# Kernel optimization log

Measured on AMD Instinct MI355X. Metric: run time of the kernel, lower is better.

The kernel has to match this reference:

```python
import jax, jax.numpy as jnp
import numpy as np
import math

B, S, DIN, DQ, DV = 8, 2048, 1024, 1024, 1024


def setup_inputs() -> dict:
    key = jax.random.key(0)
    ks = jax.random.split(key, 9)
    c_q = math.sqrt(6.0 / (DIN + DQ))
    c_v = math.sqrt(6.0 / (DIN + DV))
    query = jax.random.normal(ks[0], (B, S, DIN), dtype=jnp.float32)
    key_t = jax.random.normal(ks[1], (B, S, DIN), dtype=jnp.float32)
    value = jax.random.normal(ks[2], (B, S, DIN), dtype=jnp.float32)
    # Linear weights stored as [in, out] for x @ W; uniform init per module
    Wq = jax.random.uniform(ks[3], (DIN, DQ), jnp.float32, -c_q, c_q)
    Wk = jax.random.uniform(ks[4], (DIN, DQ), jnp.float32, -c_q, c_q)
    Wv = jax.random.uniform(ks[5], (DIN, DV), jnp.float32, -c_v, c_v)
    bq = jax.random.uniform(ks[6], (DQ,), jnp.float32, -c_q, c_q)
    bk = jax.random.uniform(ks[7], (DQ,), jnp.float32, -c_q, c_q)
    bv = jax.random.uniform(ks[8], (DV,), jnp.float32, -c_v, c_v)
    # causal mask: True where attention is disallowed (masked_fill semantics)
    mask = jnp.broadcast_to(jnp.triu(jnp.ones((S, S), dtype=bool), k=1), (B, S, S))
    return {"query": query, "key": key_t, "value": value,
            "Wq": Wq, "bq": bq, "Wk": Wk, "bk": bk, "Wv": Wv, "bv": bv,
            "mask": mask}


def reference(query, key, value, Wq, bq, Wk, bk, Wv, bv, mask):
    q = query @ Wq + bq                       # [B,S,DQ]
    k = key @ Wk + bk                         # [B,S,DQ]
    v = value @ Wv + bv                       # [B,S,DV]
    scores = jnp.einsum('bsd,btd->bst', q, k) / math.sqrt(DQ)  # [B,S,S]
    scores = jnp.where(mask, jnp.float32(-1e9), scores)
    weights = jax.nn.softmax(scores, axis=2)
    y = jnp.einsum('bst,btd->bsd', weights, v)  # [B,S,DV]
    return y
```

## Files before the change

kernel.cpp:

```cpp
#include <hip/hip_runtime.h>


typedef unsigned short u16;
typedef unsigned int   u32;
typedef float f32x4 __attribute__((ext_vector_type(4)));
typedef short s16x8 __attribute__((ext_vector_type(8)));

__device__ __forceinline__ u16 f2bf(float x) {
  u32 u = __builtin_bit_cast(u32, x);
  u += 0x7fffu + ((u >> 16) & 1u);
  return (u16)(u >> 16);
}
__device__ __forceinline__ float bf2f(u16 h) {
  u32 u = (u32)h << 16;
  return __builtin_bit_cast(float, u);
}

__device__ __forceinline__ void gld_lds16(const u16* g, u16* l) {
  __builtin_amdgcn_global_load_lds((const __attribute__((address_space(1))) void*)g,
                                   (__attribute__((address_space(3))) void*)l,
                                   16, 0, 0);
}

__global__ __launch_bounds__(256) void cvt_bf16_3(const float* __restrict__ i0,
                                                  const float* __restrict__ i1,
                                                  const float* __restrict__ i2,
                                                  u16* __restrict__ out, long X) {
  const float* in = blockIdx.y == 0 ? i0 : (blockIdx.y == 1 ? i1 : i2);
  long i = (long)blockIdx.x * 256 + threadIdx.x;
  float4 v = ((const float4*)in)[i];
  ushort4 o;
  o.x = f2bf(v.x); o.y = f2bf(v.y); o.z = f2bf(v.z); o.w = f2bf(v.w);
  ((ushort4*)(out + blockIdx.y * X))[i] = o;
}

__global__ __launch_bounds__(256) void transpose_w3(const float* __restrict__ w0,
                                                    const float* __restrict__ w1,
                                                    const float* __restrict__ w2,
                                                    u16* __restrict__ Wt,
                                                    int K, int N, long WN) {
  __shared__ u16 t[32][33];
  const float* W = blockIdx.z == 0 ? w0 : (blockIdx.z == 1 ? w1 : w2);
  u16* out = Wt + blockIdx.z * WN;
  int n0 = blockIdx.x * 32, k0 = blockIdx.y * 32;
  int tx = threadIdx.x & 31, ty = threadIdx.x >> 5;
  for (int r = ty; r < 32; r += 8)
    t[r][tx] = f2bf(W[(long)(k0 + r) * N + n0 + tx]);
  __syncthreads();
  for (int r = ty; r < 32; r += 8)
    out[(long)(n0 + r) * K + k0 + tx] = t[tx][r];
}

__global__ __launch_bounds__(256) void transpose_v(const u16* __restrict__ v,
                                                   u16* __restrict__ vt,
                                                   int S, int D) {
  __shared__ u16 t[32][33];
  long b = blockIdx.z;
  const u16* vb = v + b * S * D;
  u16* vtb = vt + b * S * D;
  int d0 = blockIdx.x * 32, s0 = blockIdx.y * 32;
  int tx = threadIdx.x & 31, ty = threadIdx.x >> 5;
  for (int r = ty; r < 32; r += 8)
    t[r][tx] = vb[(long)(s0 + r) * D + d0 + tx];
  __syncthreads();
  for (int r = ty; r < 32; r += 8)
    vtb[(long)(d0 + r) * S + s0 + tx] = t[tx][r];
}

__device__ __forceinline__ void gemm_core(const u16* __restrict__ At,
                                          const u16* __restrict__ Bt,
                                          int lda, int ldb, int ktEnd,
                                          f32x4 (&acc)[4][4],
                                          u16* lA, u16* lB) {
  const int tid = threadIdx.x;
  const int lane = tid & 63, half = lane >> 4, l16 = lane & 15;
  const int wave = tid >> 6;
  const int wm = (wave >> 1) * 64, wn = (wave & 1) * 64;

  const int c0 = tid, c1 = tid + 256;
  const int r0 = c0 >> 2, kp0 = (c0 & 3) ^ ((c0 >> 3) & 3);
  const int r1 = c1 >> 2, kp1 = (c1 & 3) ^ ((c1 >> 3) & 3);
  const u16* gA0 = At + (long)r0 * lda + kp0 * 8;
  const u16* gA1 = At + (long)r1 * lda + kp1 * 8;
  const u16* gB0 = Bt + (long)r0 * ldb + kp0 * 8;
  const u16* gB1 = Bt + (long)r1 * ldb + kp1 * 8;
  u16* lA0 = lA + c0 * 8; u16* lA1 = lA + c1 * 8;
  u16* lB0 = lB + c0 * 8; u16* lB1 = lB + c1 * 8;
  const int swz = (half ^ ((l16 >> 1) & 3)) * 8;

  for (int kt = 0; kt < ktEnd; ++kt) {
    const int k0 = kt * 32;
    gld_lds16(gA0 + k0, lA0);
    gld_lds16(gA1 + k0, lA1);
    gld_lds16(gB0 + k0, lB0);
    gld_lds16(gB1 + k0, lB1);
    __syncthreads();
    s16x8 af[4], bfr[4];
#pragma unroll
    for (int mi = 0; mi < 4; ++mi)
      af[mi] = *(const s16x8*)&lA[(wm + mi * 16 + l16) * 32 + swz];
#pragma unroll
    for (int ni = 0; ni < 4; ++ni)
      bfr[ni] = *(const s16x8*)&lB[(wn + ni * 16 + l16) * 32 + swz];
#pragma unroll
    for (int mi = 0; mi < 4; ++mi)
#pragma unroll
      for (int ni = 0; ni < 4; ++ni)
        acc[mi][ni] = __builtin_amdgcn_mfma_f32_16x16x32_bf16(af[mi], bfr[ni], acc[mi][ni], 0, 0, 0);
    __syncthreads();
  }
}

struct ProjPtrs {
  const u16* A[3];
  const u16* B[3];
  u16* C[3];
  const float* bias[3];
};

__global__ __launch_bounds__(512, 2)
void gemm_proj(ProjPtrs p) {
  const int NT = 16;
  const int NIT = 8;
  const int f = blockIdx.x;
  const int wg = (f & 7) * 96 + (f >> 3);
  const int bz = wg >> 8;
  const int rr = wg & 255;
  const int bm = rr >> 2, bn = rr & 3;

  __shared__ u16 lds[65536];
  u16* lA = lds;
  u16* lB = lds + 32768;

  const int tid = threadIdx.x;
  const int lane = tid & 63, l16 = lane & 15, lq = lane >> 4;
  const int w = tid >> 6;

  const u16* At = p.A[bz] + (long)bm * 256 * 1024;
  const u16* Bt = p.B[bz] + (long)bn * 256 * 1024;

  const int sr = tid >> 3;
  const int sc = (tid & 7) ^ (sr & 7);
  const long sO0 = (long)sr * 1024 + sc * 8;
  const int swz0 = ((lq) ^ (l16 & 7)) * 8;
  const int swz1 = ((4 + lq) ^ (l16 & 7)) * 8;
  const int aBase = (w >> 2) * 8192 + l16 * 64;
  const int bBase = ((w & 3) >> 1) * 8192 + (((w & 3) & 1) * 64 + l16) * 64;

  f32x4 acc[8][4];
#pragma unroll
  for (int i = 0; i < 8; ++i)
#pragma unroll
    for (int j = 0; j < 4; ++j) { f32x4 z = {0.f, 0.f, 0.f, 0.f}; acc[i][j] = z; }

  s16x8 af[4], bf0[4], bf1[4];

#define STG(ldsM, gM, buf, h, kt) {                               \
    u16* d_ = (ldsM) + (buf) * 16384 + (h) * 8192 + tid * 8;      \
    const u16* s_ = (gM) + (long)(h) * 131072 + (long)(kt) * 64;  \
    gld_lds16(s_ + sO0, d_);                                      \
    gld_lds16(s_ + sO0 + 65536, d_ + 4096); }
#define RD_AF(BUF, MH, SWZ)                                       \
    _Pragma("unroll") for (int mi = 0; mi < 4; ++mi)              \
      af[mi] = *(const s16x8*)&lA[(BUF) * 16384 + aBase + ((MH) * 4 + mi) * 1024 + (SWZ)];
#define RD_BF(BUF, BF, SWZ)                                       \
    _Pragma("unroll") for (int ni = 0; ni < 4; ++ni)              \
      BF[ni] = *(const s16x8*)&lB[(BUF) * 16384 + bBase + ni * 1024 + (SWZ)];
#define COMPUTE(MH, BF)                                           \
    __builtin_amdgcn_sched_barrier(0);                            \
    __builtin_amdgcn_s_barrier();                                 \
    asm volatile("s_waitcnt lgkmcnt(0)" ::: "memory");            \
    __builtin_amdgcn_sched_barrier(0);                            \
    __builtin_amdgcn_s_setprio(1);                                \
    _Pragma("unroll") for (int mi = 0; mi < 4; ++mi)              \
      _Pragma("unroll") for (int ni = 0; ni < 4; ++ni)            \
        acc[(MH) * 4 + mi][ni] = __builtin_amdgcn_mfma_f32_16x16x32_bf16(af[mi], BF[ni], acc[(MH) * 4 + mi][ni], 0, 0, 0); \
    __builtin_amdgcn_s_setprio(0);
#define ENDPH __builtin_amdgcn_s_barrier();
#define VM2 asm volatile("s_waitcnt vmcnt(2)" ::: "memory");
#define VM0 asm volatile("s_waitcnt vmcnt(0)" ::: "memory");

  STG(lB, Bt, 0, 0, 0); STG(lB, Bt, 0, 1, 0);
  STG(lA, At, 0, 0, 0); STG(lA, At, 0, 1, 0);
  STG(lB, Bt, 1, 0, 1);
  VM2;
  __builtin_amdgcn_s_barrier();

  for (int i = 0; i < NIT; ++i) {
    const int ta = 2 * i, tb = 2 * i + 1;
    const bool st = (i < NIT - 1);
    RD_AF(0, 0, swz0); RD_BF(0, bf0, swz0); STG(lB, Bt, 1, 1, tb);
    COMPUTE(0, bf0); ENDPH;
    RD_AF(0, 1, swz0); STG(lA, At, 1, 0, tb);
    COMPUTE(1, bf0); ENDPH;
    RD_AF(0, 0, swz1); RD_BF(0, bf1, swz1); STG(lA, At, 1, 1, tb);
    COMPUTE(0, bf1); ENDPH;
    RD_AF(0, 1, swz1); if (st) STG(lB, Bt, 0, 0, ta + 2);
    COMPUTE(1, bf1);
    if (st) { VM2 } else { VM0 }
    ENDPH;
    RD_AF(1, 0, swz0); RD_BF(1, bf0, swz0); if (st) STG(lB, Bt, 0, 1, ta + 2);
    COMPUTE(0, bf0); ENDPH;
    RD_AF(1, 1, swz0); if (st) STG(lA, At, 0, 0, ta + 2);
    COMPUTE(1, bf0); ENDPH;
    RD_AF(1, 0, swz1); RD_BF(1, bf1, swz1); if (st) STG(lA, At, 0, 1, ta + 2);
    COMPUTE(0, bf1); ENDPH;
    RD_AF(1, 1, swz1); if (st) STG(lB, Bt, 1, 0, tb + 2);
    COMPUTE(1, bf1);
    if (st) { VM2 }
    ENDPH;
  }
#undef STG
#undef RD_AF
#undef RD_BF
#undef COMPUTE
#undef ENDPH
#undef VM2
#undef VM0

  const int wm = (w >> 2) * 128, wn = (w & 3) * 64;
  u16* Cb = p.C[bz];
  const float* bias = p.bias[bz];
  const int colBase = bn * 256 + wn + l16;
  const long rowBase = (long)bm * 256 + wm + lq * 4;
  float bvv[4];
#pragma unroll
  for (int ni = 0; ni < 4; ++ni) bvv[ni] = bias[colBase + ni * 16];
#pragma unroll
  for (int mi = 0; mi < 8; ++mi)
#pragma unroll
    for (int ni = 0; ni < 4; ++ni) {
      const int col = colBase + ni * 16;
#pragma unroll
      for (int r = 0; r < 4; ++r)
        Cb[(rowBase + mi * 16 + r) * 1024 + col] = f2bf(acc[mi][ni][r] + bvv[ni]);
    }
}

__global__ __launch_bounds__(256, 2)
void gemm_scores_exp(const u16* __restrict__ q, const u16* __restrict__ k,
                     u16* __restrict__ E, int ld, long sQK, long sSC,
                     int kTiles, float scale) {
  const int f = blockIdx.x;
  const int bz = f & 7;
  const int t = f >> 3;
  int bm = (int)((sqrtf(8.f * t + 1.f) - 1.f) * 0.5f);
  while ((bm + 1) * (bm + 2) / 2 <= t) ++bm;
  while (bm * (bm + 1) / 2 > t) --bm;
  const int bn = t - bm * (bm + 1) / 2;

  __shared__ u16 lA[128 * 32], lB[128 * 32];
  f32x4 acc[4][4];
#pragma unroll
  for (int i = 0; i < 4; ++i)
#pragma unroll
    for (int j = 0; j < 4; ++j) { f32x4 z = {0.f, 0.f, 0.f, 0.f}; acc[i][j] = z; }

  gemm_core(q + (long)bz * sQK + (long)bm * 128 * ld,
            k + (long)bz * sQK + (long)bn * 128 * ld,
            ld, ld, kTiles, acc, lA, lB);

  const int lane = threadIdx.x & 63, half = lane >> 4, l16 = lane & 15;
  const int wave = threadIdx.x >> 6;
  const int wm = (wave >> 1) * 64, wn = (wave & 1) * 64;
  u16* Eb = E + (long)bz * sSC;
  const int colBase = bn * 128 + wn + l16;
  const int rowBase = bm * 128 + wm + half * 4;
  const bool diag = (bn == bm);
#pragma unroll
  for (int mi = 0; mi < 4; ++mi)
#pragma unroll
    for (int ni = 0; ni < 4; ++ni) {
      int col = colBase + ni * 16;
#pragma unroll
      for (int r = 0; r < 4; ++r) {
        int row = rowBase + mi * 16 + r;
        float e = __expf(acc[mi][ni][r] * scale);
        u16 out = (!diag || col <= row) ? f2bf(e) : (u16)0;
        Eb[(long)row * 2048 + col] = out;
      }
    }
}

__global__ __launch_bounds__(256) void row_inv(const u16* __restrict__ E,
                                               float* __restrict__ inv, int S) {
  const int wave = threadIdx.x >> 6, lane = threadIdx.x & 63;
  const long row = (long)blockIdx.x * 4 + wave;
  const int i = (int)(row & (S - 1));
  const int zend = ((i >> 7) + 1) << 7;
  const u16* erow = E + row * S;
  float s = 0.f;
  for (int c = lane * 4; c < zend; c += 256) {
    ushort4 u = *(const ushort4*)(erow + c);
    s += (bf2f(u.x) + bf2f(u.y)) + (bf2f(u.z) + bf2f(u.w));
  }
  for (int o = 32; o > 0; o >>= 1) s += __shfl_down(s, o);
  if (lane == 0) inv[row] = 1.f / s;
}

__global__ __launch_bounds__(256, 2)
void gemm_pv(const u16* __restrict__ E, const u16* __restrict__ vT,
             const float* __restrict__ inv, float* __restrict__ y,
             int lda, int ldb, int ldc, long sP, long sV, long sY, int S) {
  const int f = blockIdx.x;
  const int bz = f & 7;
  const int g = f >> 3;
  const int bm = 15 - (g >> 3);
  const int bn = g & 7;
  const int ktEnd = (bm + 1) * 4;

  __shared__ u16 lA[128 * 32], lB[128 * 32];
  f32x4 acc[4][4];
#pragma unroll
  for (int i = 0; i < 4; ++i)
#pragma unroll
    for (int j = 0; j < 4; ++j) { f32x4 z = {0.f, 0.f, 0.f, 0.f}; acc[i][j] = z; }

  gemm_core(E + (long)bz * sP + (long)bm * 128 * lda,
            vT + (long)bz * sV + (long)bn * 128 * ldb,
            lda, ldb, ktEnd, acc, lA, lB);

  const int lane = threadIdx.x & 63, half = lane >> 4, l16 = lane & 15;
  const int wave = threadIdx.x >> 6;
  const int wm = (wave >> 1) * 64, wn = (wave & 1) * 64;
  float* Cb = y + (long)bz * sY;
  const float* invb = inv + (long)bz * S;
  const int colBase = bn * 128 + wn + l16;
  const int rowBase = bm * 128 + wm + half * 4;
#pragma unroll
  for (int mi = 0; mi < 4; ++mi) {
    float iv[4];
#pragma unroll
    for (int r = 0; r < 4; ++r) iv[r] = invb[rowBase + mi * 16 + r];
#pragma unroll
    for (int ni = 0; ni < 4; ++ni) {
      int col = colBase + ni * 16;
#pragma unroll
      for (int r = 0; r < 4; ++r)
        Cb[(long)(rowBase + mi * 16 + r) * ldc + col] = acc[mi][ni][r] * iv[r];
    }
  }
}

extern "C" void kernel_launch(void* const* d_in, const int* in_sizes, int n_in,
                              void* d_out, int out_size, void* d_ws, size_t ws_size,
                              hipStream_t stream) {
  const int B = 8, S = 2048, DIN = 1024, DQ = 1024, DV = 1024;
  const long X  = (long)B * S * DIN;
  const long WN = (long)DIN * DQ;

  const float* query = (const float*)d_in[0];
  const float* key   = (const float*)d_in[1];
  const float* value = (const float*)d_in[2];
  const float* Wq = (const float*)d_in[3];
  const float* bq = (const float*)d_in[4];
  const float* Wk = (const float*)d_in[5];
  const float* bk = (const float*)d_in[6];
  const float* Wv = (const float*)d_in[7];
  const float* bv = (const float*)d_in[8];

  u16* w = (u16*)d_ws;
  u16* xq = w;
  u16* WT = w + 3 * X;
  const long R1 = 3 * X + 3 * WN;
  u16* vbuf = w + R1;
  u16* q  = w + R1 + X;
  u16* k  = w + R1 + 2 * X;
  u16* vT = w + R1 + 3 * X;
  u16* E = w;
  float* inv = (float*)(w + 3 * X);

  dim3 blk(256);
  cvt_bf16_3<<<dim3(X / 1024, 3), blk, 0, stream>>>(query, key, value, xq, X);
  transpose_w3<<<dim3(DQ / 32, DIN / 32, 3), blk, 0, stream>>>(Wq, Wk, Wv, WT, DIN, DQ, WN);

  ProjPtrs pp;
  pp.A[0] = xq; pp.A[1] = xq + X; pp.A[2] = xq + 2 * X;
  pp.B[0] = WT; pp.B[1] = WT + WN; pp.B[2] = WT + 2 * WN;
  pp.C[0] = q;  pp.C[1] = k;      pp.C[2] = vbuf;
  pp.bias[0] = bq; pp.bias[1] = bk; pp.bias[2] = bv;
  gemm_proj<<<dim3(768), dim3(512), 0, stream>>>(pp);

  transpose_v<<<dim3(DV / 32, S / 32, B), blk, 0, stream>>>(vbuf, vT, S, DV);

  gemm_scores_exp<<<dim3(136 * 8), blk, 0, stream>>>(
      q, k, E, DQ, X / B, (long)S * S, DQ / 32, 0.03125f);

  row_inv<<<dim3(B * S / 4), blk, 0, stream>>>(E, inv, S);

  gemm_pv<<<dim3(1024), blk, 0, stream>>>(
      E, vT, inv, (float*)d_out, S, S, DV, (long)S * S, (long)DV * S,
      (long)S * DV, S);
}
```

Baseline: 571.1 us.

## Rewrite PV GEMM as 256x128 triple-buffered async-LDS kernel with causal pairing

The P·V GEMM now uses 512-thread blocks with 256x128 output tiles, 64-wide K steps, and triple-buffered global_load_lds staging with swizzled LDS reads and priority-raised MFMA bursts. Each block handles two row tiles from opposite ends of the causal triangle to balance work. A small kernel zeroes the upper-adjacent 128-wide block of E so the coarser 256-row tiles can read past the diagonal without picking up garbage. This aims to reduce global-load latency stalls and tail imbalance, at the cost of higher LDS use and some extra K work on masked blocks.

```diff
diff --git a/kernel.cpp b/kernel.cpp
--- a/kernel.cpp
+++ b/kernel.cpp
@@ -67,6 +67,16 @@
     vtb[(long)(d0 + r) * S + s0 + tx] = t[tx][r];
 }
 
+__global__ __launch_bounds__(256) void zero_eadj(u16* __restrict__ E) {
+  const int b = blockIdx.x >> 3, i = blockIdx.x & 7;
+  u16* base = E + (long)b * 4194304 + (long)(2 * i) * 128 * 2048 + (2 * i + 1) * 128;
+  const s16x8 z = {0, 0, 0, 0, 0, 0, 0, 0};
+  for (int idx = threadIdx.x; idx < 128 * 16; idx += 256) {
+    int r = idx >> 4, c = idx & 15;
+    *(s16x8*)(base + (long)r * 2048 + c * 8) = z;
+  }
+}
+
 __device__ __forceinline__ void gemm_core(const u16* __restrict__ At,
                                           const u16* __restrict__ Bt,
                                           int lda, int ldb, int ktEnd,
@@ -120,7 +130,6 @@
 
 __global__ __launch_bounds__(512, 2)
 void gemm_proj(ProjPtrs p) {
-  const int NT = 16;
   const int NIT = 8;
   const int f = blockIdx.x;
   const int wg = (f & 7) * 96 + (f >> 3);
@@ -298,48 +307,115 @@
   if (lane == 0) inv[row] = 1.f / s;
 }
 
-__global__ __launch_bounds__(256, 2)
+__global__ __launch_bounds__(512, 2)
 void gemm_pv(const u16* __restrict__ E, const u16* __restrict__ vT,
-             const float* __restrict__ inv, float* __restrict__ y,
-             int lda, int ldb, int ldc, long sP, long sV, long sY, int S) {
+             const float* __restrict__ inv, float* __restrict__ y) {
   const int f = blockIdx.x;
   const int bz = f & 7;
   const int g = f >> 3;
-  const int bm = 15 - (g >> 3);
+  const int pr = g >> 3;
   const int bn = g & 7;
-  const int ktEnd = (bm + 1) * 4;
-
-  __shared__ u16 lA[128 * 32], lB[128 * 32];
-  f32x4 acc[4][4];
-#pragma unroll
-  for (int i = 0; i < 4; ++i)
-#pragma unroll
-    for (int j = 0; j < 4; ++j) { f32x4 z = {0.f, 0.f, 0.f, 0.f}; acc[i][j] = z; }
-
-  gemm_core(E + (long)bz * sP + (long)bm * 128 * lda,
-            vT + (long)bz * sV + (long)bn * 128 * ldb,
-            lda, ldb, ktEnd, acc, lA, lB);
-
-  const int lane = threadIdx.x & 63, half = lane >> 4, l16 = lane & 15;
-  const int wave = threadIdx.x >> 6;
-  const int wm = (wave >> 1) * 64, wn = (wave & 1) * 64;
-  float* Cb = y + (long)bz * sY;
-  const float* invb = inv + (long)bz * S;
-  const int colBase = bn * 128 + wn + l16;
-  const int rowBase = bm * 128 + wm + half * 4;
-#pragma unroll
-  for (int mi = 0; mi < 4; ++mi) {
-    float iv[4];
-#pragma unroll
-    for (int r = 0; r < 4; ++r) iv[r] = invb[rowBase + mi * 16 + r];
-#pragma unroll
-    for (int ni = 0; ni < 4; ++ni) {
-      int col = colBase + ni * 16;
-#pragma unroll
-      for (int r = 0; r < 4; ++r)
-        Cb[(long)(rowBase + mi * 16 + r) * ldc + col] = acc[mi][ni][r] * iv[r];
+
+  __shared__ u16 lds[73728];
+  u16* lA = lds;
+  u16* lB = lds + 49152;
+
+  const int tid = threadIdx.x;
+  const int lane = tid & 63, l16 = lane & 15, lq = lane >> 4;
+  const int w = tid >> 6;
+
+  const int sr = tid >> 3;
+  const int sc = (tid & 7) ^ (sr & 7);
+  const long sO = (long)sr * 2048 + sc * 8;
+
+  const int swz0 = ((lq) ^ (l16 & 7)) * 8;
+  const int swz1 = ((4 + lq) ^ (l16 & 7)) * 8;
+  const int aBase = (w >> 2) * 8192 + ((w >> 1) & 1) * 4096 + l16 * 64;
+  const int bBase = (w & 1) * 4096 + l16 * 64;
+
+  const u16* Eb = E + (long)bz * 4194304;
+  const u16* Bt = vT + (long)bz * 2097152 + (long)bn * 262144;
+  const float* invb = inv + bz * 2048;
+  float* yb = y + (long)bz * 2097152;
+
+#define PSTGA(buf, h, kt) {                                        \
+    u16* d_ = lA + (buf) * 16384 + (h) * 8192 + tid * 8;           \
+    const u16* s_ = At + (long)(h) * 262144 + (long)(kt) * 64 + sO;\
+    gld_lds16(s_, d_); gld_lds16(s_ + 131072, d_ + 4096); }
+#define PSTGB(buf, kt) {                                           \
+    u16* d_ = lB + (buf) * 8192 + tid * 8;                         \
+    const u16* s_ = Bt + (long)(kt) * 64 + sO;                     \
+    gld_lds16(s_, d_); gld_lds16(s_ + 131072, d_ + 4096); }
+#define PRD(KSWZ) {                                                \
+    _Pragma("unroll") for (int mi = 0; mi < 4; ++mi)               \
+      af[mi] = *(const s16x8*)&lA[bc * 16384 + aBase + mi * 1024 + (KSWZ)]; \
+    _Pragma("unroll") for (int ni = 0; ni < 4; ++ni)               \
+      bfr[ni] = *(const s16x8*)&lB[bc * 8192 + bBase + ni * 1024 + (KSWZ)]; }
+#define PCOMPUTE                                                   \
+    __builtin_amdgcn_sched_barrier(0);                             \
+    __builtin_amdgcn_s_barrier();                                  \
+    asm volatile("s_waitcnt lgkmcnt(0)" ::: "memory");             \
+    __builtin_amdgcn_sched_barrier(0);                             \
+    __builtin_amdgcn_s_setprio(1);                                 \
+    _Pragma("unroll") for (int mi = 0; mi < 4; ++mi)               \
+      _Pragma("unroll") for (int ni = 0; ni < 4; ++ni)             \
+        acc[mi][ni] = __builtin_amdgcn_mfma_f32_16x16x32_bf16(af[mi], bfr[ni], acc[mi][ni], 0, 0, 0); \
+    __builtin_amdgcn_s_setprio(0);
+
+  for (int hf = 0; hf < 2; ++hf) {
+    const int bm = (hf == 0) ? (7 - pr) : pr;
+    const int ktEnd = (bm + 1) * 4;
+    const u16* At = Eb + (long)bm * 524288;
+
+    f32x4 acc[4][4];
+#pragma unroll
+    for (int i = 0; i < 4; ++i)
+#pragma unroll
+      for (int j = 0; j < 4; ++j) { f32x4 z = {0.f, 0.f, 0.f, 0.f}; acc[i][j] = z; }
+
+    PSTGA(0, 0, 0); PSTGA(0, 1, 0); PSTGB(0, 0);
+    PSTGA(1, 0, 1); PSTGA(1, 1, 1); PSTGB(1, 1);
+    asm volatile("s_waitcnt vmcnt(6)" ::: "memory");
+    __builtin_amdgcn_s_barrier();
+
+    int bc = 0, bs = 2;
+    for (int u = 0; u < ktEnd; ++u) {
+      const bool st = (u + 2 < ktEnd);
+      s16x8 af[4], bfr[4];
+      PRD(swz0);
+      if (st) { PSTGA(bs, 0, u + 2); PSTGA(bs, 1, u + 2); PSTGB(bs, u + 2); }
+      PCOMPUTE;
+      __builtin_amdgcn_s_barrier();
+      PRD(swz1);
+      PCOMPUTE;
+      if (st)                  { asm volatile("s_waitcnt vmcnt(6)" ::: "memory"); }
+      else if (u == ktEnd - 2) { asm volatile("s_waitcnt vmcnt(0)" ::: "memory"); }
+      __builtin_amdgcn_s_barrier();
+      bc = (bc == 2) ? 0 : bc + 1;
+      bs = (bs == 2) ? 0 : bs + 1;
     }
+
+    const int colBase = bn * 128 + (w & 1) * 64 + l16;
+    const int rowBase = bm * 256 + (w >> 1) * 64 + lq * 4;
+#pragma unroll
+    for (int mi = 0; mi < 4; ++mi) {
+      float iv[4];
+#pragma unroll
+      for (int r = 0; r < 4; ++r) iv[r] = invb[rowBase + mi * 16 + r];
+#pragma unroll
+      for (int ni = 0; ni < 4; ++ni) {
+        const int col = colBase + ni * 16;
+#pragma unroll
+        for (int r = 0; r < 4; ++r)
+          yb[(long)(rowBase + mi * 16 + r) * 1024 + col] = acc[mi][ni][r] * iv[r];
+      }
+    }
+    __builtin_amdgcn_s_barrier();
   }
+#undef PSTGA
+#undef PSTGB
+#undef PRD
+#undef PCOMPUTE
 }
 
 extern "C" void kernel_launch(void* const* d_in, const int* in_sizes, int n_in,
@@ -383,12 +459,12 @@
 
   transpose_v<<<dim3(DV / 32, S / 32, B), blk, 0, stream>>>(vbuf, vT, S, DV);
 
+  zero_eadj<<<dim3(64), blk, 0, stream>>>(E);
+
   gemm_scores_exp<<<dim3(136 * 8), blk, 0, stream>>>(
       q, k, E, DQ, X / B, (long)S * S, DQ / 32, 0.03125f);
 
   row_inv<<<dim3(B * S / 4), blk, 0, stream>>>(E, inv, S);
 
-  gemm_pv<<<dim3(1024), blk, 0, stream>>>(
-      E, vT, inv, (float*)d_out, S, S, DV, (long)S * S, (long)DV * S,
-      (long)S * DV, S);
-}
+  gemm_pv<<<dim3(256), dim3(512), 0, stream>>>(E, vT, inv, (float*)d_out);
+}
```

New measurement: 557.2 us. 2.4% less time.
